# Kernel tuning notes

Measured on AMD Instinct MI355X. Metric: run time of the kernel, lower is better.

## Reference

```python
import jax, jax.numpy as jnp
import numpy as np

FP4_MAX = 6.0  # largest E2M1 magnitude


def _round_fp4(y):
    # Round to nearest value on the FP4 E2M1 grid {0, +-0.5, 1, 1.5, 2, 3, 4, 6}.
    a = jnp.abs(y)
    e = jnp.floor(jnp.log2(jnp.maximum(a, 1.0)))  # 0 for a<2, 1 for [2,4), 2 for >=4
    step = jnp.exp2(e - 1.0)                      # grid spacing: 0.5, 1, 2
    q = jnp.clip(jnp.round(a / step) * step, 0.0, FP4_MAX)
    return jnp.sign(y) * q


def _ste_round_fp4(y):
    # straight-through estimator: identity gradient through the rounding
    return y + jax.lax.stop_gradient(_round_fp4(y) - y)


def _mxfp4_quant(x, group_size, eps=None):
    # Groupwise MXFP4 quant-dequant along the last axis.
    lead, d = x.shape[:-1], x.shape[-1]
    g = d // group_size
    xg = x.reshape(lead + (g, group_size))
    amax = jnp.max(jnp.abs(xg), axis=-1, keepdims=True)
    # shared exponent per MX spec: floor(log2(amax)) - emax_elem (emax_elem = 2 for FP4)
    exps = jnp.where(amax > 0.0,
                     jnp.floor(jnp.log2(jnp.maximum(amax, 1e-30))) - 2.0,
                     0.0)
    scale = jnp.exp2(exps)
    if eps is not None:
        # learnable (adversarially perturbed) per-group scale epsilon
        scale = scale * (1.0 + eps[..., None])
    y = xg / scale
    xq = _ste_round_fp4(y) * scale
    return xq.reshape(x.shape), jnp.squeeze(exps, -1)


def setup_inputs() -> dict:
    key = jax.random.key(0)
    ks = jax.random.split(key, 4)
    B, S, DIN, DOUT, GS = 4, 2048, 4096, 4096, 32
    x = jax.random.normal(ks[0], (B, S, DIN), jnp.float32)
    weight_fp = jax.random.normal(ks[1], (DOUT, DIN), jnp.float32) * 0.02  # frozen FP weight
    bias = jax.random.normal(ks[2], (DOUT,), jnp.float32) * 0.01
    eps = jnp.zeros((DOUT, DIN // GS), jnp.float32)  # learnable weight-quant epsilon
    adversarial_delta = jax.random.normal(ks[3], (DOUT, DIN // GS), jnp.float32) * 0.01
    return {"x": x, "adversarial_delta": adversarial_delta,
            "weight_fp": weight_fp, "bias": bias, "eps": eps}


def reference(x, adversarial_delta, weight_fp, bias, eps):
    GS = 32
    # dynamic activation MXFP4 quantization
    x_q, act_exps = _mxfp4_quant(x, GS)
    # weight MXFP4 quantization with learnable + adversarial epsilon
    eps_eff = eps + adversarial_delta
    w_q, w_exps = _mxfp4_quant(weight_fp, GS, eps_eff)
    # F.linear(x_q, w_q, bias)
    out = jnp.einsum('bsi,oi->bso', x_q, w_q) + bias
    return (out, eps_eff, w_exps, act_exps)
```

## Files before the change

### kernel.cpp

```cpp
#include <hip/hip_runtime.h>
#include <hip/hip_bf16.h>

#define DIN   4096
#define DOUT  4096
#define MROWS 8192
#define GSIZE 32
#define NGPR  (DIN / GSIZE)
#define NG_ACT (MROWS * NGPR)
#define NG_W   (DOUT * NGPR)

typedef __bf16 bf16_t;
typedef __attribute__((ext_vector_type(8))) __bf16 bf16x8;
typedef __attribute__((ext_vector_type(4))) float f32x4;

typedef const __attribute__((address_space(1))) void* gptr_t;
typedef __attribute__((address_space(3))) void* lptr_t;

__device__ __forceinline__ float fp4_round(float y) {
  float a  = __builtin_fabsf(y);
  float am = fmaxf(a, 1.0f);
  int   e  = (int)((__float_as_uint(am) >> 23) & 255u) - 127;
  float step = __uint_as_float((unsigned)(e - 1 + 127) << 23);
  float q = rintf(a / step) * step;
  q = fminf(q, 6.0f);
  return copysignf(q, y);
}

__global__ __launch_bounds__(256) void act_quant(const float* __restrict__ x,
                                                 bf16_t* __restrict__ xq,
                                                 float* __restrict__ exps_out) {
  int g = blockIdx.x * 256 + threadIdx.x;
  const float4* xp = reinterpret_cast<const float4*>(x) + (size_t)g * 8;
  float v[32];
  float amax = 0.f;
#pragma unroll
  for (int i = 0; i < 8; ++i) {
    float4 t = xp[i];
    v[4*i+0] = t.x; v[4*i+1] = t.y; v[4*i+2] = t.z; v[4*i+3] = t.w;
    amax = fmaxf(amax, fmaxf(fmaxf(__builtin_fabsf(t.x), __builtin_fabsf(t.y)),
                             fmaxf(__builtin_fabsf(t.z), __builtin_fabsf(t.w))));
  }
  float exps = 0.f;
  if (amax > 0.f) {
    float am = fmaxf(amax, 1e-30f);
    exps = (float)((int)((__float_as_uint(am) >> 23) & 255u) - 129);
  }
  float scale = __uint_as_float((unsigned)((int)exps + 127) << 23);
  float inv   = __uint_as_float((unsigned)(127 - (int)exps) << 23);
  bf16x8 hv[4];
#pragma unroll
  for (int i = 0; i < 32; ++i) {
    float q = fp4_round(v[i] * inv) * scale;
    hv[i >> 3][i & 7] = (bf16_t)q;
  }
  bf16x8* dst = reinterpret_cast<bf16x8*>(xq + (size_t)g * 32);
#pragma unroll
  for (int i = 0; i < 4; ++i) dst[i] = hv[i];
  exps_out[g] = exps;
}

__global__ __launch_bounds__(256) void w_quant(const float* __restrict__ w,
                                               const float* __restrict__ eps,
                                               const float* __restrict__ adv,
                                               bf16_t* __restrict__ wq,
                                               float* __restrict__ eps_eff_out,
                                               float* __restrict__ w_exps_out) {
  int g = blockIdx.x * 256 + threadIdx.x;
  float ee = eps[g] + adv[g];
  eps_eff_out[g] = ee;
  const float4* wp = reinterpret_cast<const float4*>(w) + (size_t)g * 8;
  float v[32];
  float amax = 0.f;
#pragma unroll
  for (int i = 0; i < 8; ++i) {
    float4 t = wp[i];
    v[4*i+0] = t.x; v[4*i+1] = t.y; v[4*i+2] = t.z; v[4*i+3] = t.w;
    amax = fmaxf(amax, fmaxf(fmaxf(__builtin_fabsf(t.x), __builtin_fabsf(t.y)),
                             fmaxf(__builtin_fabsf(t.z), __builtin_fabsf(t.w))));
  }
  float exps = 0.f;
  if (amax > 0.f) {
    float am = fmaxf(amax, 1e-30f);
    exps = (float)((int)((__float_as_uint(am) >> 23) & 255u) - 129);
  }
  w_exps_out[g] = exps;
  float p2   = __uint_as_float((unsigned)((int)exps + 127) << 23);
  float scale = p2 * (1.0f + ee);
  bf16x8 hv[4];
#pragma unroll
  for (int i = 0; i < 32; ++i) {
    float q = fp4_round(v[i] / scale) * scale;
    hv[i >> 3][i & 7] = (bf16_t)q;
  }
  bf16x8* dst = reinterpret_cast<bf16x8*>(wq + (size_t)g * 32);
#pragma unroll
  for (int i = 0; i < 4; ++i) dst[i] = hv[i];
}

#define TILE_BYTES 32768

__global__ __launch_bounds__(512, 2) void gemm_bt(const bf16_t* __restrict__ A,
                                                  const bf16_t* __restrict__ B,
                                                  const float* __restrict__ bias,
                                                  float* __restrict__ C) {
  __shared__ bf16_t sA[2 * TILE_BYTES / 2];
  __shared__ bf16_t sB[2 * TILE_BYTES / 2];
  const int tid  = threadIdx.x;
  const int wave = tid >> 6;
  const int lane = tid & 63;

  const int swz = (blockIdx.x & 7) * 64 + (blockIdx.x >> 3);
  const int tm0 = (swz >> 4) * 256;
  const int tn0 = (swz & 15) * 256;

  const int wr = wave >> 2;
  const int wc = wave & 3;

  const int slog = ((lane & 7) ^ (lane >> 3)) * 8;
  const bf16_t* ag = A + (size_t)(tm0 + wave * 32 + (lane >> 3)) * DIN + slog;
  const bf16_t* bg = B + (size_t)(tn0 + wave * 32 + (lane >> 3)) * DIN + slog;
  const int lds_woff = wave * 32 * 64;

#define STAGE(d, kt) do {                                                          \
    const bf16_t* ap_ = ag + (kt) * 64;                                            \
    const bf16_t* bp_ = bg + (kt) * 64;                                            \
    _Pragma("unroll")                                                              \
    for (int i_ = 0; i_ < 4; ++i_) {                                               \
      __builtin_amdgcn_global_load_lds((gptr_t)(ap_ + (size_t)i_ * 8 * DIN),       \
          (lptr_t)(sA + (d) * (TILE_BYTES/2) + lds_woff + i_ * 512), 16, 0, 0);    \
      __builtin_amdgcn_global_load_lds((gptr_t)(bp_ + (size_t)i_ * 8 * DIN),       \
          (lptr_t)(sB + (d) * (TILE_BYTES/2) + lds_woff + i_ * 512), 16, 0, 0);    \
    }                                                                              \
  } while (0)

  const int arow_b = (wr * 128 + (lane & 15)) * 128;
  const int brow_b = (wc * 64  + (lane & 15)) * 128;
  const int slot0  = (((lane >> 4) ^ (lane & 7)) << 4);

  f32x4 acc[8][4] = {};

  STAGE(0, 0);
  const int NT = DIN / 64;
  for (int j = 0; j < NT; ++j) {
    const int cur = j & 1;
    if (j + 1 < NT) {
      STAGE(cur ^ 1, j + 1);
      asm volatile("s_waitcnt vmcnt(8)" ::: "memory");
    } else {
      asm volatile("s_waitcnt vmcnt(0)" ::: "memory");
    }
    asm volatile("s_barrier" ::: "memory");

    const char* bufA = (const char*)sA + cur * TILE_BYTES;
    const char* bufB = (const char*)sB + cur * TILE_BYTES;

    bf16x8 a0[4][2], a1[4][2], b0[2][2], b1[2][2];
#pragma unroll
    for (int m = 0; m < 4; ++m)
#pragma unroll
      for (int kk = 0; kk < 2; ++kk)
        a0[m][kk] = *reinterpret_cast<const bf16x8*>(bufA + arow_b + m * 2048 + (slot0 ^ (kk << 6)));
#pragma unroll
    for (int t = 0; t < 2; ++t)
#pragma unroll
      for (int kk = 0; kk < 2; ++kk) {
        b0[t][kk] = *reinterpret_cast<const bf16x8*>(bufB + brow_b + t * 2048 + (slot0 ^ (kk << 6)));
        b1[t][kk] = *reinterpret_cast<const bf16x8*>(bufB + brow_b + (2 + t) * 2048 + (slot0 ^ (kk << 6)));
      }

    __builtin_amdgcn_s_setprio(1);
#pragma unroll
    for (int kk = 0; kk < 2; ++kk)
#pragma unroll
      for (int t = 0; t < 2; ++t)
#pragma unroll
        for (int m = 0; m < 4; ++m)
          acc[m][t] = __builtin_amdgcn_mfma_f32_16x16x32_bf16(a0[m][kk], b0[t][kk], acc[m][t], 0, 0, 0);
    __builtin_amdgcn_s_setprio(0);
    asm volatile("s_barrier" ::: "memory");

#pragma unroll
    for (int m = 0; m < 4; ++m)
#pragma unroll
      for (int kk = 0; kk < 2; ++kk)
        a1[m][kk] = *reinterpret_cast<const bf16x8*>(bufA + arow_b + (4 + m) * 2048 + (slot0 ^ (kk << 6)));

    __builtin_amdgcn_s_setprio(1);
#pragma unroll
    for (int kk = 0; kk < 2; ++kk)
#pragma unroll
      for (int t = 0; t < 2; ++t)
#pragma unroll
        for (int m = 0; m < 4; ++m)
          acc[m][2 + t] = __builtin_amdgcn_mfma_f32_16x16x32_bf16(a0[m][kk], b1[t][kk], acc[m][2 + t], 0, 0, 0);
    __builtin_amdgcn_s_setprio(0);
    asm volatile("s_barrier" ::: "memory");

    __builtin_amdgcn_s_setprio(1);
#pragma unroll
    for (int kk = 0; kk < 2; ++kk)
#pragma unroll
      for (int t = 0; t < 2; ++t)
#pragma unroll
        for (int m = 0; m < 4; ++m)
          acc[4 + m][t] = __builtin_amdgcn_mfma_f32_16x16x32_bf16(a1[m][kk], b0[t][kk], acc[4 + m][t], 0, 0, 0);
    __builtin_amdgcn_s_setprio(0);
    asm volatile("s_barrier" ::: "memory");

    __builtin_amdgcn_s_setprio(1);
#pragma unroll
    for (int kk = 0; kk < 2; ++kk)
#pragma unroll
      for (int t = 0; t < 2; ++t)
#pragma unroll
        for (int m = 0; m < 4; ++m)
          acc[4 + m][2 + t] = __builtin_amdgcn_mfma_f32_16x16x32_bf16(a1[m][kk], b1[t][kk], acc[4 + m][2 + t], 0, 0, 0);
    __builtin_amdgcn_s_setprio(0);
    asm volatile("s_barrier" ::: "memory");
  }

  const int r0 = tm0 + wr * 128 + ((lane >> 4) << 2);
  const int c0 = tn0 + wc * 64 + (lane & 15);
#pragma unroll
  for (int n = 0; n < 4; ++n) {
    float bv = bias[c0 + n * 16];
#pragma unroll
    for (int m = 0; m < 8; ++m) {
#pragma unroll
      for (int jj = 0; jj < 4; ++jj) {
        C[(size_t)(r0 + m * 16 + jj) * DOUT + c0 + n * 16] = acc[m][n][jj] + bv;
      }
    }
  }
#undef STAGE
}

extern "C" void kernel_launch(void* const* d_in, const int* in_sizes, int n_in,
                              void* d_out, int out_size, void* d_ws, size_t ws_size,
                              hipStream_t stream) {
  const float* x    = (const float*)d_in[0];
  const float* adv  = (const float*)d_in[1];
  const float* wfp  = (const float*)d_in[2];
  const float* bias = (const float*)d_in[3];
  const float* eps  = (const float*)d_in[4];

  float* out      = (float*)d_out;
  float* eps_eff  = out + (size_t)MROWS * DOUT;
  float* w_exps   = eps_eff + NG_W;
  float* act_exps = w_exps + NG_W;

  bf16_t* xq = (bf16_t*)d_ws;
  bf16_t* wq = (bf16_t*)d_ws + (size_t)MROWS * DIN;

  act_quant<<<NG_ACT / 256, 256, 0, stream>>>(x, xq, act_exps);
  w_quant<<<NG_W / 256, 256, 0, stream>>>(wfp, eps, adv, wq, eps_eff, w_exps);
  gemm_bt<<<dim3((MROWS / 256) * (DOUT / 256)), 512, 0, stream>>>(xq, wq, bias, out);
}
```

Measured before the change: 389.1 us.

## Prefetch two K-tiles ahead with staggered per-half loads into freed buffers

Restructures the GEMM main loop to keep two K-tiles in flight. Loads of tile j+2 are issued into the current buffer once its B and A fragments have been read into registers. The global-to-LDS loads are split into halves and interleaved between the MFMA phases, and B fragments are loaded lazily per half. The aim is to hide global memory latency better and spread load issue across compute. In exchange there are more barriers and explicit lgkmcnt waits, and the synchronisation is more fragile.

```diff
diff --git a/kernel.cpp b/kernel.cpp
--- a/kernel.cpp
+++ b/kernel.cpp
@@ -97,14 +97,14 @@
   for (int i = 0; i < 4; ++i) dst[i] = hv[i];
 }
 
-#define TILE_BYTES 32768
+#define NT 64
 
 __global__ __launch_bounds__(512, 2) void gemm_bt(const bf16_t* __restrict__ A,
                                                   const bf16_t* __restrict__ B,
                                                   const float* __restrict__ bias,
                                                   float* __restrict__ C) {
-  __shared__ bf16_t sA[2 * TILE_BYTES / 2];
-  __shared__ bf16_t sB[2 * TILE_BYTES / 2];
+  __shared__ bf16_t sA[2 * 16384];
+  __shared__ bf16_t sB[2 * 16384];
   const int tid  = threadIdx.x;
   const int wave = tid >> 6;
   const int lane = tid & 63;
@@ -116,107 +116,122 @@
   const int wr = wave >> 2;
   const int wc = wave & 3;
 
-  const int slog = ((lane & 7) ^ (lane >> 3)) * 8;
-  const bf16_t* ag = A + (size_t)(tm0 + wave * 32 + (lane >> 3)) * DIN + slog;
-  const bf16_t* bg = B + (size_t)(tn0 + wave * 32 + (lane >> 3)) * DIN + slog;
-  const int lds_woff = wave * 32 * 64;
-
-#define STAGE(d, kt) do {                                                          \
-    const bf16_t* ap_ = ag + (kt) * 64;                                            \
-    const bf16_t* bp_ = bg + (kt) * 64;                                            \
-    _Pragma("unroll")                                                              \
-    for (int i_ = 0; i_ < 4; ++i_) {                                               \
-      __builtin_amdgcn_global_load_lds((gptr_t)(ap_ + (size_t)i_ * 8 * DIN),       \
-          (lptr_t)(sA + (d) * (TILE_BYTES/2) + lds_woff + i_ * 512), 16, 0, 0);    \
-      __builtin_amdgcn_global_load_lds((gptr_t)(bp_ + (size_t)i_ * 8 * DIN),       \
-          (lptr_t)(sB + (d) * (TILE_BYTES/2) + lds_woff + i_ * 512), 16, 0, 0);    \
-    }                                                                              \
+  const int lrow8 = lane >> 3;
+  const int csw   = ((lane & 7) ^ lrow8) * 8;
+  const bf16_t* gA = A + (size_t)(tm0 + wave * 16 + lrow8) * DIN + csw;
+  const bf16_t* gB = B + (size_t)(tn0 + wave * 16 + lrow8) * DIN + csw;
+  const int stg0 = wave * 1024;
+
+#define STGH(sM, gM, d, h, kt) do {                                          \
+    const bf16_t* g_ = (gM) + (size_t)(h) * 128 * DIN + (size_t)(kt) * 64;   \
+    __builtin_amdgcn_global_load_lds((gptr_t)g_,                             \
+        (lptr_t)((sM) + (d) * 16384 + (h) * 8192 + stg0), 16, 0, 0);         \
+    __builtin_amdgcn_global_load_lds((gptr_t)(g_ + 8 * DIN),                 \
+        (lptr_t)((sM) + (d) * 16384 + (h) * 8192 + stg0 + 512), 16, 0, 0);   \
   } while (0)
 
   const int arow_b = (wr * 128 + (lane & 15)) * 128;
-  const int brow_b = (wc * 64  + (lane & 15)) * 128;
+  const int brow_b = (wc * 64 + (lane & 15)) * 128;
   const int slot0  = (((lane >> 4) ^ (lane & 7)) << 4);
 
   f32x4 acc[8][4] = {};
 
-  STAGE(0, 0);
-  const int NT = DIN / 64;
+  STGH(sA, gA, 0, 0, 0); STGH(sA, gA, 0, 1, 0);
+  STGH(sB, gB, 0, 0, 0); STGH(sB, gB, 0, 1, 0);
+  STGH(sB, gB, 1, 0, 1); STGH(sB, gB, 1, 1, 1);
+  STGH(sA, gA, 1, 0, 1); STGH(sA, gA, 1, 1, 1);
+  asm volatile("s_waitcnt vmcnt(8)" ::: "memory");
+  asm volatile("s_barrier" ::: "memory");
+
   for (int j = 0; j < NT; ++j) {
-    const int cur = j & 1;
-    if (j + 1 < NT) {
-      STAGE(cur ^ 1, j + 1);
+    const int p = j & 1;
+    const char* bufA = (const char*)sA + p * 32768;
+    const char* bufB = (const char*)sB + p * 32768;
+    bf16x8 a0[4][2], a1[4][2], bn[4][2];
+
+#pragma unroll
+    for (int m = 0; m < 4; ++m)
+#pragma unroll
+      for (int kk = 0; kk < 2; ++kk)
+        a0[m][kk] = *reinterpret_cast<const bf16x8*>(bufA + arow_b + m * 2048 + (slot0 ^ (kk << 6)));
+#pragma unroll
+    for (int t = 0; t < 2; ++t)
+#pragma unroll
+      for (int kk = 0; kk < 2; ++kk)
+        bn[t][kk] = *reinterpret_cast<const bf16x8*>(bufB + brow_b + t * 2048 + (slot0 ^ (kk << 6)));
+    asm volatile("s_barrier" ::: "memory");
+    asm volatile("s_waitcnt lgkmcnt(0)" ::: "memory");
+    __builtin_amdgcn_s_setprio(1);
+#pragma unroll
+    for (int kk = 0; kk < 2; ++kk)
+#pragma unroll
+      for (int t = 0; t < 2; ++t)
+#pragma unroll
+        for (int m = 0; m < 4; ++m)
+          acc[m][t] = __builtin_amdgcn_mfma_f32_16x16x32_bf16(a0[m][kk], bn[t][kk], acc[m][t], 0, 0, 0);
+    __builtin_amdgcn_s_setprio(0);
+    asm volatile("s_barrier" ::: "memory");
+
+#pragma unroll
+    for (int t = 2; t < 4; ++t)
+#pragma unroll
+      for (int kk = 0; kk < 2; ++kk)
+        bn[t][kk] = *reinterpret_cast<const bf16x8*>(bufB + brow_b + t * 2048 + (slot0 ^ (kk << 6)));
+    asm volatile("s_barrier" ::: "memory");
+    asm volatile("s_waitcnt lgkmcnt(0)" ::: "memory");
+    __builtin_amdgcn_s_setprio(1);
+#pragma unroll
+    for (int kk = 0; kk < 2; ++kk)
+#pragma unroll
+      for (int t = 0; t < 2; ++t)
+#pragma unroll
+        for (int m = 0; m < 4; ++m)
+          acc[m][2 + t] = __builtin_amdgcn_mfma_f32_16x16x32_bf16(a0[m][kk], bn[2 + t][kk], acc[m][2 + t], 0, 0, 0);
+    __builtin_amdgcn_s_setprio(0);
+    asm volatile("s_barrier" ::: "memory");
+
+#pragma unroll
+    for (int m = 0; m < 4; ++m)
+#pragma unroll
+      for (int kk = 0; kk < 2; ++kk)
+        a1[m][kk] = *reinterpret_cast<const bf16x8*>(bufA + arow_b + (4 + m) * 2048 + (slot0 ^ (kk << 6)));
+    if (j + 2 < NT) {
+      STGH(sB, gB, p, 0, j + 2);
+      STGH(sB, gB, p, 1, j + 2);
+    }
+    asm volatile("s_barrier" ::: "memory");
+    asm volatile("s_waitcnt lgkmcnt(0)" ::: "memory");
+    __builtin_amdgcn_s_setprio(1);
+#pragma unroll
+    for (int kk = 0; kk < 2; ++kk)
+#pragma unroll
+      for (int t = 0; t < 2; ++t)
+#pragma unroll
+        for (int m = 0; m < 4; ++m)
+          acc[4 + m][t] = __builtin_amdgcn_mfma_f32_16x16x32_bf16(a1[m][kk], bn[t][kk], acc[4 + m][t], 0, 0, 0);
+    __builtin_amdgcn_s_setprio(0);
+    asm volatile("s_barrier" ::: "memory");
+
+    if (j + 2 < NT) {
+      STGH(sA, gA, p, 0, j + 2);
+      STGH(sA, gA, p, 1, j + 2);
+    }
+    asm volatile("s_barrier" ::: "memory");
+    __builtin_amdgcn_s_setprio(1);
+#pragma unroll
+    for (int kk = 0; kk < 2; ++kk)
+#pragma unroll
+      for (int t = 0; t < 2; ++t)
+#pragma unroll
+        for (int m = 0; m < 4; ++m)
+          acc[4 + m][2 + t] = __builtin_amdgcn_mfma_f32_16x16x32_bf16(a1[m][kk], bn[2 + t][kk], acc[4 + m][2 + t], 0, 0, 0);
+    __builtin_amdgcn_s_setprio(0);
+    if (j < NT - 2) {
       asm volatile("s_waitcnt vmcnt(8)" ::: "memory");
     } else {
       asm volatile("s_waitcnt vmcnt(0)" ::: "memory");
     }
     asm volatile("s_barrier" ::: "memory");
-
-    const char* bufA = (const char*)sA + cur * TILE_BYTES;
-    const char* bufB = (const char*)sB + cur * TILE_BYTES;
-
-    bf16x8 a0[4][2], a1[4][2], b0[2][2], b1[2][2];
-#pragma unroll
-    for (int m = 0; m < 4; ++m)
-#pragma unroll
-      for (int kk = 0; kk < 2; ++kk)
-        a0[m][kk] = *reinterpret_cast<const bf16x8*>(bufA + arow_b + m * 2048 + (slot0 ^ (kk << 6)));
-#pragma unroll
-    for (int t = 0; t < 2; ++t)
-#pragma unroll
-      for (int kk = 0; kk < 2; ++kk) {
-        b0[t][kk] = *reinterpret_cast<const bf16x8*>(bufB + brow_b + t * 2048 + (slot0 ^ (kk << 6)));
-        b1[t][kk] = *reinterpret_cast<const bf16x8*>(bufB + brow_b + (2 + t) * 2048 + (slot0 ^ (kk << 6)));
-      }
-
-    __builtin_amdgcn_s_setprio(1);
-#pragma unroll
-    for (int kk = 0; kk < 2; ++kk)
-#pragma unroll
-      for (int t = 0; t < 2; ++t)
-#pragma unroll
-        for (int m = 0; m < 4; ++m)
-          acc[m][t] = __builtin_amdgcn_mfma_f32_16x16x32_bf16(a0[m][kk], b0[t][kk], acc[m][t], 0, 0, 0);
-    __builtin_amdgcn_s_setprio(0);
-    asm volatile("s_barrier" ::: "memory");
-
-#pragma unroll
-    for (int m = 0; m < 4; ++m)
-#pragma unroll
-      for (int kk = 0; kk < 2; ++kk)
-        a1[m][kk] = *reinterpret_cast<const bf16x8*>(bufA + arow_b + (4 + m) * 2048 + (slot0 ^ (kk << 6)));
-
-    __builtin_amdgcn_s_setprio(1);
-#pragma unroll
-    for (int kk = 0; kk < 2; ++kk)
-#pragma unroll
-      for (int t = 0; t < 2; ++t)
-#pragma unroll
-        for (int m = 0; m < 4; ++m)
-          acc[m][2 + t] = __builtin_amdgcn_mfma_f32_16x16x32_bf16(a0[m][kk], b1[t][kk], acc[m][2 + t], 0, 0, 0);
-    __builtin_amdgcn_s_setprio(0);
-    asm volatile("s_barrier" ::: "memory");
-
-    __builtin_amdgcn_s_setprio(1);
-#pragma unroll
-    for (int kk = 0; kk < 2; ++kk)
-#pragma unroll
-      for (int t = 0; t < 2; ++t)
-#pragma unroll
-        for (int m = 0; m < 4; ++m)
-          acc[4 + m][t] = __builtin_amdgcn_mfma_f32_16x16x32_bf16(a1[m][kk], b0[t][kk], acc[4 + m][t], 0, 0, 0);
-    __builtin_amdgcn_s_setprio(0);
-    asm volatile("s_barrier" ::: "memory");
-
-    __builtin_amdgcn_s_setprio(1);
-#pragma unroll
-    for (int kk = 0; kk < 2; ++kk)
-#pragma unroll
-      for (int t = 0; t < 2; ++t)
-#pragma unroll
-        for (int m = 0; m < 4; ++m)
-          acc[4 + m][2 + t] = __builtin_amdgcn_mfma_f32_16x16x32_bf16(a1[m][kk], b1[t][kk], acc[4 + m][2 + t], 0, 0, 0);
-    __builtin_amdgcn_s_setprio(0);
-    asm volatile("s_barrier" ::: "memory");
   }
 
   const int r0 = tm0 + wr * 128 + ((lane >> 4) << 2);
@@ -232,7 +247,7 @@
       }
     }
   }
-#undef STAGE
+#undef STGH
 }
 
 extern "C" void kernel_launch(void* const* d_in, const int* in_sizes, int n_in,
```

Measured after the change: 352.1 us. 9.5% less time.
